# Optimization experiments

Hardware: AMD Instinct MI355X
Metric: run time of the kernel (lower is better)

The kernel has to match this reference:

```python
import jax, jax.numpy as jnp
import numpy as np
from itertools import product

_N = 50000
_G = 52  # voxel grid extent


def _build_maps():
    rs = np.random.RandomState(0)
    ids = rs.choice(_G ** 3, size=_N, replace=False)
    coords = np.stack(np.unravel_index(ids, (_G, _G, _G)), axis=1)  # [N,3]
    order = np.argsort(ids)
    sorted_ids = ids[order]
    in_lists, out_lists = [], []
    for off in product((-1, 0, 1), repeat=3):
        nb = coords + np.array(off)
        valid = np.all((nb >= 0) & (nb < _G), axis=1)
        nb_id = nb[:, 0] * _G * _G + nb[:, 1] * _G + nb[:, 2]
        pos = np.searchsorted(sorted_ids, nb_id)
        pos_c = np.minimum(pos, _N - 1)
        found = valid & (sorted_ids[pos_c] == nb_id)
        in_lists.append(order[pos_c[found]].astype(np.int32))
        out_lists.append(np.nonzero(found)[0].astype(np.int32))
    P = max(len(a) for a in in_lists)  # identity offset -> P == N
    K = len(in_lists)
    in_idx = np.full((K, P), _N, dtype=np.int32)   # sentinel = zero row
    out_idx = np.full((K, P), _N, dtype=np.int32)  # sentinel = dummy out row
    for k in range(K):
        in_idx[k, : len(in_lists[k])] = in_lists[k]
        out_idx[k, : len(out_lists[k])] = out_lists[k]
    pid = (coords[:, 0] // 2) * 26 * 26 + (coords[:, 1] // 2) * 26 + (coords[:, 2] // 2)
    uniq, inv = np.unique(pid, return_inverse=True)
    return in_idx, out_idx, inv.astype(np.int32), int(len(uniq))


def setup_inputs() -> dict:
    key = jax.random.key(0)
    ks = jax.random.split(key, 10)
    in_idx, out_idx, pool_idx, num_pool = _build_maps()
    s1 = 1.0 / np.sqrt(27 * 256)
    s2 = 1.0 / np.sqrt(27 * 512)
    return {
        "feats": jax.random.normal(ks[0], (_N, 256), jnp.float32),
        "W1": jax.random.normal(ks[1], (27, 256, 512), jnp.float32) * s1,
        "g1": 1.0 + 0.1 * jax.random.normal(ks[2], (512,), jnp.float32),
        "b1": 0.05 * jax.random.normal(ks[3], (512,), jnp.float32),
        "W2": jax.random.normal(ks[4], (27, 512, 512), jnp.float32) * s2,
        "g2": 1.0 + 0.1 * jax.random.normal(ks[5], (512,), jnp.float32),
        "b2": 0.05 * jax.random.normal(ks[6], (512,), jnp.float32),
        "W3": jax.random.normal(ks[7], (27, 512, 512), jnp.float32) * s2,
        "g3": 1.0 + 0.1 * jax.random.normal(ks[8], (512,), jnp.float32),
        "b3": 0.05 * jax.random.normal(ks[9], (512,), jnp.float32),
        "in_idx": jnp.asarray(in_idx),
        "out_idx": jnp.asarray(out_idx),
        "pool_idx": jnp.asarray(pool_idx),
        "num_pool": num_pool,
    }


def _sparse_conv(feats, W, in_idx, out_idx):
    # gather-GEMM-scatter over K=27 kernel offsets (MinkowskiConvolution)
    N, Cin = feats.shape
    fp = jnp.concatenate([feats, jnp.zeros((1, Cin), feats.dtype)], axis=0)
    acc0 = jnp.zeros((N + 1, W.shape[-1]), feats.dtype)  # last row = dummy sink
    def step(acc, xs):
        ii, oi, Wk = xs
        return acc.at[oi].add(fp[ii] @ Wk), None
    acc, _ = jax.lax.scan(step, acc0, (in_idx, out_idx, W))
    return acc[:N]


def _bn_relu(x, g, b, eps=1e-5):
    m = x.mean(axis=0)
    v = x.var(axis=0)  # biased, matching torch BN normalization
    return jax.nn.relu((x - m) * jax.lax.rsqrt(v + eps) * g + b)


def reference(feats, W1, g1, b1, W2, g2, b2, W3, g3, b3, in_idx, out_idx, pool_idx, num_pool):
    x = _bn_relu(_sparse_conv(feats, W1, in_idx, out_idx), g1, b1)
    x = _bn_relu(_sparse_conv(x, W2, in_idx, out_idx), g2, b2)
    x = _bn_relu(_sparse_conv(x, W3, in_idx, out_idx), g3, b3)
    return jax.ops.segment_max(x, pool_idx, num_segments=num_pool)
```

## Files before the change

kernel.cpp:

```cpp
#include <hip/hip_runtime.h>
#include <hip/hip_bf16.h>
#include <stdint.h>

typedef __attribute__((ext_vector_type(8))) short bf16x8;
typedef __attribute__((ext_vector_type(4))) float f32x4;
typedef unsigned short u16;

__device__ __forceinline__ u16 f2bf(float x) {
  unsigned u = __float_as_uint(x);
  unsigned r = (u + 0x7FFFu + ((u >> 16) & 1u)) >> 16;
  return (u16)r;
}

__device__ __forceinline__ void gl_lds16(const void* g, void* l) {
  __builtin_amdgcn_global_load_lds((const __attribute__((address_space(1))) void*)g,
                                   (__attribute__((address_space(3))) void*)l, 16, 0, 0);
}


__global__ void zero_i32_kernel(int* p, int n) {
  int i = blockIdx.x * blockDim.x + threadIdx.x;
  if (i < n) p[i] = 0;
}

__global__ void init_nbr_kernel(int* nbr, int total, int N) {
  for (int i = blockIdx.x * blockDim.x + threadIdx.x; i < total; i += gridDim.x * blockDim.x)
    nbr[i] = N;
}

__global__ void scatter_nbr_kernel(const int* __restrict__ in_idx, const int* __restrict__ out_idx,
                                   int* __restrict__ nbr, int N, int P, int NPAD) {
  const int total = 27 * P;
  for (int i = blockIdx.x * blockDim.x + threadIdx.x; i < total; i += gridDim.x * blockDim.x) {
    const int o = out_idx[i];
    if ((unsigned)o < (unsigned)N) {
      const int k = i / P;
      nbr[(size_t)k * NPAD + o] = in_idx[i];
    }
  }
}

__global__ void cvt_feats_kernel(const float* __restrict__ F, u16* __restrict__ X0, int N) {
  const int total = (N + 1) * 64;
  for (int i = blockIdx.x * blockDim.x + threadIdx.x; i < total; i += gridDim.x * blockDim.x) {
    const int r = i >> 6;
    ushort4 o;
    if (r < N) {
      const float4 v = ((const float4*)F)[i];
      o.x = f2bf(v.x); o.y = f2bf(v.y); o.z = f2bf(v.z); o.w = f2bf(v.w);
    } else {
      o.x = 0; o.y = 0; o.z = 0; o.w = 0;
    }
    ((ushort4*)X0)[i] = o;
  }
}

__global__ void cvt_w_kernel(const float* __restrict__ W, u16* __restrict__ Wt, int CIN) {
  __shared__ float t[32][33];
  const int k = blockIdx.z;
  const int c0 = blockIdx.y * 32;
  const int n0 = blockIdx.x * 32;
  const int tx = threadIdx.x, ty = threadIdx.y;
  const float* Wk = W + (size_t)k * CIN * 512;
  for (int i = ty; i < 32; i += 8)
    t[i][tx] = Wk[(size_t)(c0 + i) * 512 + n0 + tx];
  __syncthreads();
  u16* Wtk = Wt + (size_t)k * 512 * CIN;
  for (int i = ty; i < 32; i += 8)
    Wtk[(size_t)(n0 + i) * CIN + c0 + tx] = f2bf(t[tx][i]);
}


__global__ void scatter_members_kernel(const int* __restrict__ pool_idx, int* __restrict__ gcnt,
                                       int* __restrict__ mlist, int N) {
  const int r = blockIdx.x * blockDim.x + threadIdx.x;
  if (r < N) {
    const int p = pool_idx[r];
    const int pos = atomicAdd(&gcnt[p], 1);
    if (pos < 8) mlist[p * 8 + pos] = r;
  }
}

__global__ void pool_grouped_kernel(const float* __restrict__ Y, const float* __restrict__ sc,
                                    const float* __restrict__ sh, const int* __restrict__ gcnt,
                                    const int* __restrict__ mlist, float* __restrict__ out) {
  const int p = blockIdx.x;
  const int t = threadIdx.x;
  const int c = t * 2;
  const float s0 = sc[c], s1 = sc[c + 1];
  const float h0 = sh[c], h1 = sh[c + 1];
  int n = gcnt[p];
  if (n > 8) n = 8;
  float m0 = 0.f, m1 = 0.f;
  for (int i = 0; i < n; ++i) {
    const int r = mlist[p * 8 + i];
    const float2 v = *(const float2*)&Y[(size_t)r * 512 + c];
    m0 = fmaxf(m0, fmaxf(fmaf(v.x, s0, h0), 0.f));
    m1 = fmaxf(m1, fmaxf(fmaf(v.y, s1, h1), 0.f));
  }
  float2 o; o.x = m0; o.y = m1;
  *(float2*)&out[(size_t)p * 512 + c] = o;
}


template <int CIN>
__global__ __launch_bounds__(256, 2) void conv_kernel(
    const u16* __restrict__ X,
    const u16* __restrict__ Wt,
    const int* __restrict__ nbr,
    float* __restrict__ Y,
    int N, int NPAD) {
  constexpr int KK = CIN / 32;
  constexpr int NSTEPS = 27 * KK;
  __shared__ __align__(16) u16 lds[16384];

  const int tid = threadIdx.x;
  const int lane = tid & 63;
  const int wv = tid >> 6;
  const int wm = wv >> 1, wn = wv & 1;
  const int row0 = (blockIdx.x >> 2) * 128;
  const int col0 = (blockIdx.x & 3) * 128;

  const int sc = tid & 3;
  int srow[2], scs[2];
  size_t boffg[2];
#pragma unroll
  for (int i = 0; i < 2; ++i) {
    srow[i] = i * 64 + (tid >> 2);
    scs[i] = (sc ^ ((srow[i] >> 1) & 3)) * 8;
    boffg[i] = (size_t)(col0 + srow[i]) * CIN + scs[i];
  }

  const int lr = lane & 15;
  const int q = lane >> 4;
  int aoff[4], boff[4];
#pragma unroll
  for (int f = 0; f < 4; ++f) {
    const int ra = wm * 64 + f * 16 + lr;
    aoff[f] = ra * 32 + ((q ^ ((ra >> 1) & 3)) * 8);
    const int rb = wn * 64 + f * 16 + lr;
    boff[f] = 4096 + rb * 32 + ((q ^ ((rb >> 1) & 3)) * 8);
  }

  f32x4 acc[4][4];
#pragma unroll
  for (int a = 0; a < 4; ++a)
#pragma unroll
    for (int b = 0; b < 4; ++b) acc[a][b] = (f32x4){0.f, 0.f, 0.f, 0.f};

  size_t arow[2];
#pragma unroll
  for (int i = 0; i < 2; ++i) arow[i] = (size_t)nbr[row0 + srow[i]] * CIN;

#pragma unroll
  for (int i = 0; i < 2; ++i) {
    gl_lds16(X + arow[i] + scs[i], &lds[i * 2048 + wv * 512]);
    gl_lds16(Wt + boffg[i], &lds[4096 + i * 2048 + wv * 512]);
  }

  int cur = 0;
  for (int s = 0; s < NSTEPS; ++s) {
    __syncthreads();
    const int ns = s + 1;
    if (ns < NSTEPS) {
      const int k = ns / KK;
      const int kk = ns % KK;
      if (kk == 0) {
        const int* nb = nbr + (size_t)k * NPAD + row0;
#pragma unroll
        for (int i = 0; i < 2; ++i) arow[i] = (size_t)nb[srow[i]] * CIN;
      }
      const int nxt = cur ^ 1;
      const int ko = kk * 32;
      const size_t kb = (size_t)k * (512 * CIN);
#pragma unroll
      for (int i = 0; i < 2; ++i) {
        gl_lds16(X + arow[i] + ko + scs[i], &lds[nxt * 8192 + i * 2048 + wv * 512]);
        gl_lds16(Wt + kb + boffg[i] + ko, &lds[nxt * 8192 + 4096 + i * 2048 + wv * 512]);
      }
    }
    const u16* lb = &lds[cur * 8192];
    bf16x8 av[4], bv[4];
#pragma unroll
    for (int f = 0; f < 4; ++f) av[f] = *(const bf16x8*)&lb[aoff[f]];
#pragma unroll
    for (int f = 0; f < 4; ++f) bv[f] = *(const bf16x8*)&lb[boff[f]];
#pragma unroll
    for (int a = 0; a < 4; ++a)
#pragma unroll
      for (int b = 0; b < 4; ++b)
        acc[a][b] = __builtin_amdgcn_mfma_f32_16x16x32_bf16(av[a], bv[b], acc[a][b], 0, 0, 0);
    cur ^= 1;
  }

#pragma unroll
  for (int a = 0; a < 4; ++a) {
    const int r0 = row0 + wm * 64 + a * 16 + q * 4;
#pragma unroll
    for (int b = 0; b < 4; ++b) {
      const int c = col0 + wn * 64 + b * 16 + lr;
#pragma unroll
      for (int j = 0; j < 4; ++j) {
        const int r = r0 + j;
        if (r < N) Y[(size_t)r * 512 + c] = acc[a][b][j];
      }
    }
  }
}


__global__ void bn_stats_kernel(const float* __restrict__ Y, float* __restrict__ st, int N) {
  const int t = threadIdx.x;
  float s0 = 0.f, s1 = 0.f, q0 = 0.f, q1 = 0.f;
  for (int r = blockIdx.x; r < N; r += gridDim.x) {
    const float2 v = *(const float2*)&Y[(size_t)r * 512 + t * 2];
    s0 += v.x; s1 += v.y; q0 += v.x * v.x; q1 += v.y * v.y;
  }
  atomicAdd(&st[2 * t], s0);
  atomicAdd(&st[2 * t + 1], s1);
  atomicAdd(&st[512 + 2 * t], q0);
  atomicAdd(&st[512 + 2 * t + 1], q1);
}

__global__ void bn_finalize_kernel(const float* __restrict__ st, const float* __restrict__ g,
                                   const float* __restrict__ b, float* __restrict__ sc,
                                   float* __restrict__ sh, int N) {
  const int c = threadIdx.x;
  if (c < 512) {
    const float inv = 1.f / (float)N;
    const float m = st[c] * inv;
    const float v = st[512 + c] * inv - m * m;
    const float rs = rsqrtf(v + 1e-5f);
    const float s = rs * g[c];
    sc[c] = s;
    sh[c] = b[c] - m * s;
  }
}

__global__ void bn_norm_kernel(const float* __restrict__ Y, const float* __restrict__ sc,
                               const float* __restrict__ sh, u16* __restrict__ Xn, int N) {
  const int total = (N + 1) * 128;
  for (int i = blockIdx.x * blockDim.x + threadIdx.x; i < total; i += gridDim.x * blockDim.x) {
    const int r = i >> 7;
    const int c = (i & 127) * 4;
    ushort4 o;
    if (r < N) {
      const float4 y = *(const float4*)&Y[(size_t)r * 512 + c];
      const float v0 = fmaxf(fmaf(y.x, sc[c + 0], sh[c + 0]), 0.f);
      const float v1 = fmaxf(fmaf(y.y, sc[c + 1], sh[c + 1]), 0.f);
      const float v2 = fmaxf(fmaf(y.z, sc[c + 2], sh[c + 2]), 0.f);
      const float v3 = fmaxf(fmaf(y.w, sc[c + 3], sh[c + 3]), 0.f);
      o.x = f2bf(v0); o.y = f2bf(v1); o.z = f2bf(v2); o.w = f2bf(v3);
    } else {
      o.x = 0; o.y = 0; o.z = 0; o.w = 0;
    }
    *(ushort4*)&Xn[(size_t)r * 512 + c] = o;
  }
}


extern "C" void kernel_launch(void* const* d_in, const int* in_sizes, int n_in,
                              void* d_out, int out_size, void* d_ws, size_t ws_size,
                              hipStream_t stream) {
  const float* feats = (const float*)d_in[0];
  const float* W1 = (const float*)d_in[1];
  const float* g1 = (const float*)d_in[2];
  const float* b1 = (const float*)d_in[3];
  const float* W2 = (const float*)d_in[4];
  const float* g2 = (const float*)d_in[5];
  const float* b2 = (const float*)d_in[6];
  const float* W3 = (const float*)d_in[7];
  const float* g3 = (const float*)d_in[8];
  const float* b3 = (const float*)d_in[9];
  const int* in_idx = (const int*)d_in[10];
  const int* out_idx = (const int*)d_in[11];
  const int* pool_idx = (const int*)d_in[12];
  float* out = (float*)d_out;

  const int N = in_sizes[0] / 256;
  const int P = in_sizes[10] / 27;
  const int NPAD = ((N + 127) / 128) * 128;
  const int npool = out_size / 512;
  (void)n_in; (void)ws_size;

  char* w = (char*)d_ws;
  size_t off = 0;
  auto carve = [&](size_t bytes) {
    void* p = w + off;
    off += (bytes + 511) & ~(size_t)511;
    return p;
  };
  u16* X0 = (u16*)carve((size_t)(N + 1) * 256 * 2);
  u16* X1 = (u16*)carve((size_t)(N + 1) * 512 * 2);
  float* Y = (float*)carve((size_t)N * 512 * 4);
  u16* W1t = (u16*)carve((size_t)27 * 512 * 256 * 2);
  u16* W2t = (u16*)carve((size_t)27 * 512 * 512 * 2);
  u16* W3t = (u16*)carve((size_t)27 * 512 * 512 * 2);
  float* st0 = (float*)carve(1024 * 4);
  float* st1 = (float*)carve(1024 * 4);
  float* st2 = (float*)carve(1024 * 4);
  float* sc = (float*)carve(512 * 4);
  float* sh = (float*)carve(512 * 4);
  int* nbr = (int*)carve((size_t)27 * NPAD * 4);

  int* gcnt = (int*)X0;
  int* mlist = (int*)((char*)X0 + (1 << 17));

  const int convGrid = (NPAD / 128) * 4;

  zero_i32_kernel<<<4, 256, 0, stream>>>((int*)st0, 1024);
  zero_i32_kernel<<<4, 256, 0, stream>>>((int*)st1, 1024);
  zero_i32_kernel<<<4, 256, 0, stream>>>((int*)st2, 1024);
  init_nbr_kernel<<<2048, 256, 0, stream>>>(nbr, 27 * NPAD, N);
  scatter_nbr_kernel<<<2048, 256, 0, stream>>>(in_idx, out_idx, nbr, N, P, NPAD);
  cvt_feats_kernel<<<2048, 256, 0, stream>>>(feats, X0, N);
  cvt_w_kernel<<<dim3(16, 8, 27), dim3(32, 8), 0, stream>>>(W1, W1t, 256);
  cvt_w_kernel<<<dim3(16, 16, 27), dim3(32, 8), 0, stream>>>(W2, W2t, 512);
  cvt_w_kernel<<<dim3(16, 16, 27), dim3(32, 8), 0, stream>>>(W3, W3t, 512);

  conv_kernel<256><<<convGrid, 256, 0, stream>>>(X0, W1t, nbr, Y, N, NPAD);
  zero_i32_kernel<<<(npool + 255) / 256, 256, 0, stream>>>(gcnt, npool);
  scatter_members_kernel<<<(N + 255) / 256, 256, 0, stream>>>(pool_idx, gcnt, mlist, N);
  bn_stats_kernel<<<512, 256, 0, stream>>>(Y, st0, N);
  bn_finalize_kernel<<<1, 512, 0, stream>>>(st0, g1, b1, sc, sh, N);
  bn_norm_kernel<<<4096, 256, 0, stream>>>(Y, sc, sh, X1, N);

  conv_kernel<512><<<convGrid, 256, 0, stream>>>(X1, W2t, nbr, Y, N, NPAD);
  bn_stats_kernel<<<512, 256, 0, stream>>>(Y, st1, N);
  bn_finalize_kernel<<<1, 512, 0, stream>>>(st1, g2, b2, sc, sh, N);
  bn_norm_kernel<<<4096, 256, 0, stream>>>(Y, sc, sh, X1, N);

  conv_kernel<512><<<convGrid, 256, 0, stream>>>(X1, W3t, nbr, Y, N, NPAD);
  bn_stats_kernel<<<512, 256, 0, stream>>>(Y, st2, N);
  bn_finalize_kernel<<<1, 512, 0, stream>>>(st2, g3, b3, sc, sh, N);
  pool_grouped_kernel<<<npool, 256, 0, stream>>>(Y, sc, sh, gcnt, mlist, out);
}
```

Baseline: 1.940 ms.

## Use 256x256 tiles with 4-stage LDS pipeline in sparse conv GEMM

Replaces the 128x128, 4-wave conv kernel with a 256x256-tile, 8-wave kernel that runs a 4-slot LDS ring, interleaving half-tile loads with MFMA groups. It adds explicit vmcnt waits, sched barriers and setprio, prefetches neighbor indices several steps ahead, and remaps block IDs across XCDs. The aim is more operand reuse per byte of gathered activation and weight, and better hiding of global-load latency. The trade-off is far more LDS (128KB) and accumulator registers per block, which lowers occupancy, and fewer blocks to fill the GPU.

```diff
diff --git a/kernel.cpp b/kernel.cpp
--- a/kernel.cpp
+++ b/kernel.cpp
@@ -104,105 +104,168 @@
 
 
 template <int CIN>
-__global__ __launch_bounds__(256, 2) void conv_kernel(
+__global__ __launch_bounds__(512, 2) void conv256_kernel(
     const u16* __restrict__ X,
     const u16* __restrict__ Wt,
     const int* __restrict__ nbr,
     float* __restrict__ Y,
     int N, int NPAD) {
-  constexpr int KK = CIN / 32;
-  constexpr int NSTEPS = 27 * KK;
-  __shared__ __align__(16) u16 lds[16384];
+  constexpr int KKT = CIN / 64;
+  constexpr int NT = 27 * KKT;
+  __shared__ __align__(16) u16 lds[65536];
+  u16* As = lds;
+  u16* Bs = lds + 32768;
 
   const int tid = threadIdx.x;
   const int lane = tid & 63;
   const int wv = tid >> 6;
-  const int wm = wv >> 1, wn = wv & 1;
-  const int row0 = (blockIdx.x >> 2) * 128;
-  const int col0 = (blockIdx.x & 3) * 128;
-
-  const int sc = tid & 3;
-  int srow[2], scs[2];
-  size_t boffg[2];
-#pragma unroll
-  for (int i = 0; i < 2; ++i) {
-    srow[i] = i * 64 + (tid >> 2);
-    scs[i] = (sc ^ ((srow[i] >> 1) & 3)) * 8;
-    boffg[i] = (size_t)(col0 + srow[i]) * CIN + scs[i];
-  }
-
+  const int wr = wv >> 2;
+  const int wc = wv & 3;
   const int lr = lane & 15;
   const int q = lane >> 4;
-  int aoff[4], boff[4];
-#pragma unroll
-  for (int f = 0; f < 4; ++f) {
-    const int ra = wm * 64 + f * 16 + lr;
-    aoff[f] = ra * 32 + ((q ^ ((ra >> 1) & 3)) * 8);
-    const int rb = wn * 64 + f * 16 + lr;
-    boff[f] = 4096 + rb * 32 + ((q ^ ((rb >> 1) & 3)) * 8);
-  }
-
-  f32x4 acc[4][4];
-#pragma unroll
-  for (int a = 0; a < 4; ++a)
-#pragma unroll
-    for (int b = 0; b < 4; ++b) acc[a][b] = (f32x4){0.f, 0.f, 0.f, 0.f};
-
-  size_t arow[2];
-#pragma unroll
-  for (int i = 0; i < 2; ++i) arow[i] = (size_t)nbr[row0 + srow[i]] * CIN;
-
-#pragma unroll
-  for (int i = 0; i < 2; ++i) {
-    gl_lds16(X + arow[i] + scs[i], &lds[i * 2048 + wv * 512]);
-    gl_lds16(Wt + boffg[i], &lds[4096 + i * 2048 + wv * 512]);
-  }
-
-  int cur = 0;
-  for (int s = 0; s < NSTEPS; ++s) {
-    __syncthreads();
-    const int ns = s + 1;
-    if (ns < NSTEPS) {
-      const int k = ns / KK;
-      const int kk = ns % KK;
-      if (kk == 0) {
-        const int* nb = nbr + (size_t)k * NPAD + row0;
-#pragma unroll
-        for (int i = 0; i < 2; ++i) arow[i] = (size_t)nb[srow[i]] * CIN;
-      }
-      const int nxt = cur ^ 1;
-      const int ko = kk * 32;
-      const size_t kb = (size_t)k * (512 * CIN);
-#pragma unroll
-      for (int i = 0; i < 2; ++i) {
-        gl_lds16(X + arow[i] + ko + scs[i], &lds[nxt * 8192 + i * 2048 + wv * 512]);
-        gl_lds16(Wt + kb + boffg[i] + ko, &lds[nxt * 8192 + 4096 + i * 2048 + wv * 512]);
-      }
-    }
-    const u16* lb = &lds[cur * 8192];
-    bf16x8 av[4], bv[4];
-#pragma unroll
-    for (int f = 0; f < 4; ++f) av[f] = *(const bf16x8*)&lb[aoff[f]];
-#pragma unroll
-    for (int f = 0; f < 4; ++f) bv[f] = *(const bf16x8*)&lb[boff[f]];
-#pragma unroll
-    for (int a = 0; a < 4; ++a)
-#pragma unroll
-      for (int b = 0; b < 4; ++b)
-        acc[a][b] = __builtin_amdgcn_mfma_f32_16x16x32_bf16(av[a], bv[b], acc[a][b], 0, 0, 0);
-    cur ^= 1;
-  }
-
-#pragma unroll
-  for (int a = 0; a < 4; ++a) {
-    const int r0 = row0 + wm * 64 + a * 16 + q * 4;
-#pragma unroll
-    for (int b = 0; b < 4; ++b) {
-      const int c = col0 + wn * 64 + b * 16 + lr;
+
+  int bid = blockIdx.x;
+  if ((gridDim.x & 7) == 0) {
+    const int cpx = gridDim.x >> 3;
+    bid = (bid & 7) * cpx + (bid >> 3);
+  }
+  const int row0 = (bid >> 1) * 256;
+  const int colbase = (bid & 1) * 256;
+
+  const int srow = tid >> 2;
+  const int csrc = (((tid & 3) ^ ((tid >> 3) & 3)) * 8);
+  const int swz8 = (q ^ ((lr >> 1) & 3)) * 8;
+  const int aoffL = (wr * 128 + lr) * 32 + swz8;
+  const int boffL = (wc * 64 + lr) * 32 + swz8;
+
+  f32x4 acc[8][4];
+#pragma unroll
+  for (int m = 0; m < 8; ++m)
+#pragma unroll
+    for (int n = 0; n < 4; ++n) acc[m][n] = (f32x4){0.f, 0.f, 0.f, 0.f};
+
+  auto stageA = [&](int slot, int tt, int kk, int nb0, int nb1) {
+    const int ko = (tt % KKT) * 64 + kk * 32;
+    gl_lds16(X + (size_t)nb0 * CIN + ko + csrc, &As[slot * 8192 + wv * 512]);
+    gl_lds16(X + (size_t)nb1 * CIN + ko + csrc, &As[slot * 8192 + 4096 + wv * 512]);
+  };
+  auto stageB = [&](int slot, int tt, int kk) {
+    const int k27 = tt / KKT;
+    const int ko = (tt % KKT) * 64 + kk * 32;
+    const u16* base = Wt + (size_t)k27 * (512 * CIN) + ko + csrc;
+    gl_lds16(base + (size_t)(colbase + srow) * CIN, &Bs[slot * 8192 + wv * 512]);
+    gl_lds16(base + (size_t)(colbase + 128 + srow) * CIN, &Bs[slot * 8192 + 4096 + wv * 512]);
+  };
+  auto loadnbr0 = [&](int tt) {
+    int t2 = (tt < NT - 1) ? tt : (NT - 1);
+    const volatile int* p = nbr + (size_t)(t2 / KKT) * NPAD + row0 + srow;
+    return p[0];
+  };
+  auto loadnbr1 = [&](int tt) {
+    int t2 = (tt < NT - 1) ? tt : (NT - 1);
+    const volatile int* p = nbr + (size_t)(t2 / KKT) * NPAD + row0 + 128 + srow;
+    return p[0];
+  };
+
+  bf16x8 a[4], b[4];
+
+  int nbC0 = loadnbr0(0), nbC1 = loadnbr1(0);
+  int nbN0 = nbC0, nbN1 = nbC1;
+  stageA(0, 0, 0, nbC0, nbC1);
+  stageB(0, 0, 0);
+  stageA(1, 0, 1, nbC0, nbC1);
+  stageB(1, 0, 1);
+  stageA(2, 1, 0, nbC0, nbC1);
+  stageB(2, 1, 0);
+
+  for (int t = 0; t < NT; ++t) {
+    const int s0 = (2 * t) & 3;
+    const int s1 = (2 * t + 1) & 3;
+    const u16* as0 = As + s0 * 8192;
+    const u16* bs0 = Bs + s0 * 8192;
+    const u16* as1 = As + s1 * 8192;
+    const u16* bs1 = Bs + s1 * 8192;
+
+    if (t < NT - 1) asm volatile("s_waitcnt vmcnt(8)" ::: "memory");
+    else            asm volatile("s_waitcnt vmcnt(0)" ::: "memory");
+    __builtin_amdgcn_s_barrier();
+    asm volatile("" ::: "memory");
+#pragma unroll
+    for (int m = 0; m < 4; ++m) a[m] = *(const bf16x8*)&as0[aoffL + m * 512];
+#pragma unroll
+    for (int n = 0; n < 4; ++n) b[n] = *(const bf16x8*)&bs0[boffL + n * 512];
+    __builtin_amdgcn_sched_barrier(0);
+    if (t + 1 < NT) stageA((2 * t + 3) & 3, t + 1, 1, nbC0, nbC1);
+    __builtin_amdgcn_sched_barrier(0);
+    __builtin_amdgcn_s_setprio(1);
+#pragma unroll
+    for (int m = 0; m < 4; ++m)
+#pragma unroll
+      for (int n = 0; n < 4; ++n)
+        acc[m][n] = __builtin_amdgcn_mfma_f32_16x16x32_bf16(a[m], b[n], acc[m][n], 0, 0, 0);
+    __builtin_amdgcn_s_setprio(0);
+
+#pragma unroll
+    for (int m = 0; m < 4; ++m) a[m] = *(const bf16x8*)&as0[aoffL + (m + 4) * 512];
+    __builtin_amdgcn_sched_barrier(0);
+    if (t + 1 < NT) stageB((2 * t + 3) & 3, t + 1, 1);
+    __builtin_amdgcn_sched_barrier(0);
+    __builtin_amdgcn_s_setprio(1);
+#pragma unroll
+    for (int m = 0; m < 4; ++m)
+#pragma unroll
+      for (int n = 0; n < 4; ++n)
+        acc[m + 4][n] = __builtin_amdgcn_mfma_f32_16x16x32_bf16(a[m], b[n], acc[m + 4][n], 0, 0, 0);
+    __builtin_amdgcn_s_setprio(0);
+
+    if (t < NT - 1) asm volatile("s_waitcnt vmcnt(8)" ::: "memory");
+    else            asm volatile("s_waitcnt vmcnt(0)" ::: "memory");
+    __builtin_amdgcn_s_barrier();
+    asm volatile("" ::: "memory");
+#pragma unroll
+    for (int m = 0; m < 4; ++m) a[m] = *(const bf16x8*)&as1[aoffL + m * 512];
+#pragma unroll
+    for (int n = 0; n < 4; ++n) b[n] = *(const bf16x8*)&bs1[boffL + n * 512];
+    __builtin_amdgcn_sched_barrier(0);
+    if (t + 2 < NT) stageA(s0, t + 2, 0, nbN0, nbN1);
+    const int nbF0 = loadnbr0(t + 3);
+    const int nbF1 = loadnbr1(t + 3);
+    __builtin_amdgcn_sched_barrier(0);
+    __builtin_amdgcn_s_setprio(1);
+#pragma unroll
+    for (int m = 0; m < 4; ++m)
+#pragma unroll
+      for (int n = 0; n < 4; ++n)
+        acc[m][n] = __builtin_amdgcn_mfma_f32_16x16x32_bf16(a[m], b[n], acc[m][n], 0, 0, 0);
+    __builtin_amdgcn_s_setprio(0);
+
+#pragma unroll
+    for (int m = 0; m < 4; ++m) a[m] = *(const bf16x8*)&as1[aoffL + (m + 4) * 512];
+    __builtin_amdgcn_sched_barrier(0);
+    if (t + 2 < NT) stageB(s0, t + 2, 0);
+    __builtin_amdgcn_sched_barrier(0);
+    __builtin_amdgcn_s_setprio(1);
+#pragma unroll
+    for (int m = 0; m < 4; ++m)
+#pragma unroll
+      for (int n = 0; n < 4; ++n)
+        acc[m + 4][n] = __builtin_amdgcn_mfma_f32_16x16x32_bf16(a[m], b[n], acc[m + 4][n], 0, 0, 0);
+    __builtin_amdgcn_s_setprio(0);
+
+    nbC0 = nbN0; nbC1 = nbN1;
+    nbN0 = nbF0; nbN1 = nbF1;
+  }
+
+#pragma unroll
+  for (int m = 0; m < 8; ++m) {
+    const int r0 = row0 + wr * 128 + m * 16 + q * 4;
+#pragma unroll
+    for (int n = 0; n < 4; ++n) {
+      const int c = colbase + wc * 64 + n * 16 + lr;
 #pragma unroll
       for (int j = 0; j < 4; ++j) {
         const int r = r0 + j;
-        if (r < N) Y[(size_t)r * 512 + c] = acc[a][b][j];
+        if (r < N) Y[(size_t)r * 512 + c] = acc[m][n][j];
       }
     }
   }
@@ -279,7 +342,7 @@
 
   const int N = in_sizes[0] / 256;
   const int P = in_sizes[10] / 27;
-  const int NPAD = ((N + 127) / 128) * 128;
+  const int NPAD = ((N + 255) / 256) * 256;
   const int npool = out_size / 512;
   (void)n_in; (void)ws_size;
 
@@ -306,7 +369,7 @@
   int* gcnt = (int*)X0;
   int* mlist = (int*)((char*)X0 + (1 << 17));
 
-  const int convGrid = (NPAD / 128) * 4;
+  const int convGrid = (NPAD / 256) * 2;
 
   zero_i32_kernel<<<4, 256, 0, stream>>>((int*)st0, 1024);
   zero_i32_kernel<<<4, 256, 0, stream>>>((int*)st1, 1024);
@@ -318,19 +381,19 @@
   cvt_w_kernel<<<dim3(16, 16, 27), dim3(32, 8), 0, stream>>>(W2, W2t, 512);
   cvt_w_kernel<<<dim3(16, 16, 27), dim3(32, 8), 0, stream>>>(W3, W3t, 512);
 
-  conv_kernel<256><<<convGrid, 256, 0, stream>>>(X0, W1t, nbr, Y, N, NPAD);
+  conv256_kernel<256><<<convGrid, 512, 0, stream>>>(X0, W1t, nbr, Y, N, NPAD);
   zero_i32_kernel<<<(npool + 255) / 256, 256, 0, stream>>>(gcnt, npool);
   scatter_members_kernel<<<(N + 255) / 256, 256, 0, stream>>>(pool_idx, gcnt, mlist, N);
   bn_stats_kernel<<<512, 256, 0, stream>>>(Y, st0, N);
   bn_finalize_kernel<<<1, 512, 0, stream>>>(st0, g1, b1, sc, sh, N);
   bn_norm_kernel<<<4096, 256, 0, stream>>>(Y, sc, sh, X1, N);
 
-  conv_kernel<512><<<convGrid, 256, 0, stream>>>(X1, W2t, nbr, Y, N, NPAD);
+  conv256_kernel<512><<<convGrid, 512, 0, stream>>>(X1, W2t, nbr, Y, N, NPAD);
   bn_stats_kernel<<<512, 256, 0, stream>>>(Y, st1, N);
   bn_finalize_kernel<<<1, 512, 0, stream>>>(st1, g2, b2, sc, sh, N);
   bn_norm_kernel<<<4096, 256, 0, stream>>>(Y, sc, sh, X1, N);
 
-  conv_kernel<512><<<convGrid, 256, 0, stream>>>(X1, W3t, nbr, Y, N, NPAD);
+  conv256_kernel<512><<<convGrid, 512, 0, stream>>>(X1, W3t, nbr, Y, N, NPAD);
   bn_stats_kernel<<<512, 256, 0, stream>>>(Y, st2, N);
   bn_finalize_kernel<<<1, 512, 0, stream>>>(st2, g3, b3, sc, sh, N);
   pool_grouped_kernel<<<npool, 256, 0, stream>>>(Y, sc, sh, gcnt, mlist, out);
```

Result: slower. 2.181 ms (+12.4%).

## Fuse BN statistics into conv epilogue and remap blocks across XCDs

Applied to the files above, without the earlier changes.

Batch-norm sum and sum-of-squares are now accumulated in the conv kernel epilogue from the register accumulators. They are reduced with wave shuffles and LDS atomics, then pushed to global with atomics, so the separate bn_stats pass that reread the whole 50000x512 fp32 output three times is removed. Block IDs are also remapped so that consecutive tiles land on the same XCD chiplet, aiming for better L2 reuse of the weight and neighbour data. The cost is extra epilogue work and global atomics per block, and the summation order changes.

```diff
diff --git a/kernel.cpp b/kernel.cpp
--- a/kernel.cpp
+++ b/kernel.cpp
@@ -109,6 +109,7 @@
     const u16* __restrict__ Wt,
     const int* __restrict__ nbr,
     float* __restrict__ Y,
+    float* __restrict__ st,
     int N, int NPAD) {
   constexpr int KK = CIN / 32;
   constexpr int NSTEPS = 27 * KK;
@@ -118,8 +119,14 @@
   const int lane = tid & 63;
   const int wv = tid >> 6;
   const int wm = wv >> 1, wn = wv & 1;
-  const int row0 = (blockIdx.x >> 2) * 128;
-  const int col0 = (blockIdx.x & 3) * 128;
+
+  int bid = blockIdx.x;
+  if ((gridDim.x & 7) == 0) {
+    const int cpx = gridDim.x >> 3;
+    bid = (bid & 7) * cpx + (bid >> 3);
+  }
+  const int row0 = (bid >> 2) * 128;
+  const int col0 = (bid & 3) * 128;
 
   const int sc = tid & 3;
   int srow[2], scs[2];
@@ -206,21 +213,40 @@
       }
     }
   }
-}
-
-
-__global__ void bn_stats_kernel(const float* __restrict__ Y, float* __restrict__ st, int N) {
-  const int t = threadIdx.x;
-  float s0 = 0.f, s1 = 0.f, q0 = 0.f, q1 = 0.f;
-  for (int r = blockIdx.x; r < N; r += gridDim.x) {
-    const float2 v = *(const float2*)&Y[(size_t)r * 512 + t * 2];
-    s0 += v.x; s1 += v.y; q0 += v.x * v.x; q1 += v.y * v.y;
-  }
-  atomicAdd(&st[2 * t], s0);
-  atomicAdd(&st[2 * t + 1], s1);
-  atomicAdd(&st[512 + 2 * t], q0);
-  atomicAdd(&st[512 + 2 * t + 1], q1);
-}
+
+  __syncthreads();
+  float* fls = (float*)lds;
+  if (tid < 256) fls[tid] = 0.f;
+  __syncthreads();
+#pragma unroll
+  for (int b = 0; b < 4; ++b) {
+    float s = 0.f, q2 = 0.f;
+#pragma unroll
+    for (int a = 0; a < 4; ++a) {
+      const int rbase = row0 + wm * 64 + a * 16 + q * 4;
+#pragma unroll
+      for (int j = 0; j < 4; ++j) {
+        if (rbase + j < N) {
+          const float v = acc[a][b][j];
+          s += v; q2 += v * v;
+        }
+      }
+    }
+    s += __shfl_xor(s, 16);  s += __shfl_xor(s, 32);
+    q2 += __shfl_xor(q2, 16); q2 += __shfl_xor(q2, 32);
+    if (q == 0) {
+      const int cl = wn * 64 + b * 16 + lr;
+      atomicAdd(&fls[cl], s);
+      atomicAdd(&fls[128 + cl], q2);
+    }
+  }
+  __syncthreads();
+  if (tid < 128) {
+    atomicAdd(&st[col0 + tid], fls[tid]);
+    atomicAdd(&st[512 + col0 + tid], fls[128 + tid]);
+  }
+}
+
 
 __global__ void bn_finalize_kernel(const float* __restrict__ st, const float* __restrict__ g,
                                    const float* __restrict__ b, float* __restrict__ sc,
@@ -318,20 +344,17 @@
   cvt_w_kernel<<<dim3(16, 16, 27), dim3(32, 8), 0, stream>>>(W2, W2t, 512);
   cvt_w_kernel<<<dim3(16, 16, 27), dim3(32, 8), 0, stream>>>(W3, W3t, 512);
 
-  conv_kernel<256><<<convGrid, 256, 0, stream>>>(X0, W1t, nbr, Y, N, NPAD);
+  conv_kernel<256><<<convGrid, 256, 0, stream>>>(X0, W1t, nbr, Y, st0, N, NPAD);
   zero_i32_kernel<<<(npool + 255) / 256, 256, 0, stream>>>(gcnt, npool);
   scatter_members_kernel<<<(N + 255) / 256, 256, 0, stream>>>(pool_idx, gcnt, mlist, N);
-  bn_stats_kernel<<<512, 256, 0, stream>>>(Y, st0, N);
   bn_finalize_kernel<<<1, 512, 0, stream>>>(st0, g1, b1, sc, sh, N);
   bn_norm_kernel<<<4096, 256, 0, stream>>>(Y, sc, sh, X1, N);
 
-  conv_kernel<512><<<convGrid, 256, 0, stream>>>(X1, W2t, nbr, Y, N, NPAD);
-  bn_stats_kernel<<<512, 256, 0, stream>>>(Y, st1, N);
+  conv_kernel<512><<<convGrid, 256, 0, stream>>>(X1, W2t, nbr, Y, st1, N, NPAD);
   bn_finalize_kernel<<<1, 512, 0, stream>>>(st1, g2, b2, sc, sh, N);
   bn_norm_kernel<<<4096, 256, 0, stream>>>(Y, sc, sh, X1, N);
 
-  conv_kernel<512><<<convGrid, 256, 0, stream>>>(X1, W3t, nbr, Y, N, NPAD);
-  bn_stats_kernel<<<512, 256, 0, stream>>>(Y, st2, N);
+  conv_kernel<512><<<convGrid, 256, 0, stream>>>(X1, W3t, nbr, Y, st2, N, NPAD);
   bn_finalize_kernel<<<1, 512, 0, stream>>>(st2, g3, b3, sc, sh, N);
   pool_grouped_kernel<<<npool, 256, 0, stream>>>(Y, sc, sh, gcnt, mlist, out);
 }
```

New measurement: 1.807 ms. 6.9% less time.
